# Kernel optimization log

Measured on AMD Instinct MI355X. Metric: run time of the kernel, lower is better.

The kernel has to match this reference:

```python
import jax, jax.numpy as jnp
import numpy as np
import math

B, L, E, H = 512, 200, 64, 4
D = E // H
NEG = jnp.float32(-(2.0 ** 32) + 1.0)


def setup_inputs() -> dict:
    key = jax.random.key(0)
    ks = jax.random.split(key, 12)
    inp = jax.random.normal(ks[0], (B, L, E), dtype=jnp.float32)
    # realistic variable-length histories: mask[b, t] = t < len_b, len_b in [1, L]
    lens = jax.random.randint(ks[1], (B, 1), 1, L + 1)
    mask = jnp.arange(L)[None, :] < lens  # [B, L] bool
    s = 1.0 / math.sqrt(E)
    pos_enc = jax.random.normal(ks[2], (1, L, E), dtype=jnp.float32)
    Wk = jax.random.uniform(ks[3], (E, E), jnp.float32, -s, s)
    bk = jnp.zeros((E,), jnp.float32)
    Wv = jax.random.uniform(ks[4], (E, E), jnp.float32, -s, s)
    bv = jnp.zeros((E,), jnp.float32)
    Wq = jax.random.uniform(ks[5], (E, E), jnp.float32, -s, s)
    bq = jnp.zeros((E,), jnp.float32)
    Wf = jax.random.uniform(ks[6], (E, E), jnp.float32, -s, s)
    bf = jnp.zeros((E,), jnp.float32)
    return {"input": inp, "mask": mask, "pos_enc": pos_enc,
            "Wk": Wk, "bk": bk, "Wv": Wv, "bv": bv,
            "Wq": Wq, "bq": bq, "Wf": Wf, "bf": bf}


def reference(input, mask, pos_enc, Wk, bk, Wv, bv, Wq, bq, Wf, bf):
    x = input + pos_enc  # [B, L, E]
    # project and split heads: [B, H, L, D]
    def split(t):
        return t.reshape(B, L, H, D).transpose(0, 2, 1, 3)
    k = split(x @ Wk.T + bk)
    v = split(x @ Wv.T + bv)
    q = split(x @ Wq.T + bq) / math.sqrt(D)
    scores = jnp.einsum('bhqd,bhkd->bhqk', q, k)  # [B, H, L, L]
    # key_mask in torch code broadcasts over dim 3 (mask on the QUERY axis),
    # query_mask is its transpose (mask on the KEY axis). Combined: both must be valid.
    both = mask[:, None, :, None] & mask[:, None, None, :]  # [B, 1, L, L]
    scores = jnp.where(both, scores, NEG)
    attn = jax.nn.softmax(scores, axis=-1)
    # dropout is identity at inference; omitted deterministically
    out = jnp.einsum('bhqk,bhkd->bhqd', attn, v)
    out = out.transpose(0, 2, 1, 3).reshape(B, L, E)
    out = out @ Wf.T + bf
    fm = mask.astype(jnp.float32)[:, :, None]  # [B, L, 1]
    lens = jnp.sum(fm, axis=1)  # [B, 1]
    pooled = jnp.sum(out * fm, axis=1) / (lens + 1e-8)  # [B, E]
    return pooled
```

## Files before the change

### kernel.cpp

```cpp
#include <hip/hip_runtime.h>
#include <hip/hip_fp16.h>
#include <math.h>

#define Bn 512
#define Ln 200
#define En 64
#define Hn 4
#define Dn 16
#define KS3 18
#define VS3 200
#define QSC 0.36067376022224085f

typedef _Float16 __f16;
typedef __f16 f16x4 __attribute__((ext_vector_type(4)));
typedef __f16 f16x8 __attribute__((ext_vector_type(8)));
typedef float f32x4 __attribute__((ext_vector_type(4)));

#if __has_builtin(__builtin_amdgcn_exp2f)
__device__ __forceinline__ float fexp2(float x) { return __builtin_amdgcn_exp2f(x); }
#else
__device__ __forceinline__ float fexp2(float x) { return exp2f(x); }
#endif

__device__ __forceinline__ f16x8 pack8s(float4 a, float4 b, float4 pa, float4 pb) {
    f16x8 r;
    r[0] = (__f16)(a.x + pa.x); r[1] = (__f16)(a.y + pa.y);
    r[2] = (__f16)(a.z + pa.z); r[3] = (__f16)(a.w + pa.w);
    r[4] = (__f16)(b.x + pb.x); r[5] = (__f16)(b.y + pb.y);
    r[6] = (__f16)(b.z + pb.z); r[7] = (__f16)(b.w + pb.w);
    return r;
}
__device__ __forceinline__ f16x8 pack8(float4 a, float4 b) {
    f16x8 r;
    r[0] = (__f16)a.x; r[1] = (__f16)a.y; r[2] = (__f16)a.z; r[3] = (__f16)a.w;
    r[4] = (__f16)b.x; r[5] = (__f16)b.y; r[6] = (__f16)b.z; r[7] = (__f16)b.w;
    return r;
}

__global__ __launch_bounds__(256, 4) void fused_kernel(
    const float* __restrict__ input, const int* __restrict__ mask,
    const float* __restrict__ pos_enc,
    const float* __restrict__ Wk, const float* __restrict__ bk,
    const float* __restrict__ Wv, const float* __restrict__ bv,
    const float* __restrict__ Wq, const float* __restrict__ bq,
    const float* __restrict__ Wf, const float* __restrict__ bf_,
    float* __restrict__ out)
{
    __shared__ __align__(16) __f16 Kh[Ln * KS3];
    __shared__ __align__(16) __f16 Qh[Ln * KS3];
    __shared__ __align__(16) __f16 Vt[16 * VS3];
    __shared__ float lred[4][4][16];
    __shared__ float red[4][16];
    __shared__ float ph[16];
    __shared__ int cnt_red[4];

    const int tid  = threadIdx.x;
    const int b    = blockIdx.x >> 2, h = blockIdx.x & 3;
    const int wave = tid >> 6, lane = tid & 63;
    const int quad = lane >> 4, ln16 = lane & 15;

    const int mv = (tid < Ln) ? mask[b * Ln + tid] : 0;

    f16x8 bfr[3][2];
    #pragma unroll
    for (int m = 0; m < 3; ++m) {
        const float* W = (m == 0) ? Wk : (m == 1) ? Wv : Wq;
        #pragma unroll
        for (int ks = 0; ks < 2; ++ks) {
            const float4* wp = (const float4*)(W + (size_t)(h * 16 + ln16) * 64) + (ks * 8 + quad * 2);
            bfr[m][ks] = pack8(wp[0], wp[1]);
        }
    }
    const int cg = h * 16 + ln16;
    const float bkv = bk[cg], bvv = bv[cg], bqv = bq[cg];

    int c = (mv != 0) ? 1 : 0;
    #pragma unroll
    for (int off = 32; off; off >>= 1) c += __shfl_down(c, off, 64);
    if (lane == 0) cnt_red[wave] = c;
    __syncthreads();
    const int len = cnt_red[0] + cnt_red[1] + cnt_red[2] + cnt_red[3];
    const int nt = (len + 15) >> 4;

    const float4* in4 = (const float4*)(input + (size_t)b * Ln * En);
    const float4* pe4 = (const float4*)pos_enc;

    for (int rt = wave; rt < nt; rt += 4) {
        const int R = rt * 16 + ln16;
        const bool rok = (R < Ln);
        f16x8 af[2];
        #pragma unroll
        for (int ks = 0; ks < 2; ++ks) {
            float4 xa = {0,0,0,0}, xb = {0,0,0,0}, pa = {0,0,0,0}, pb = {0,0,0,0};
            if (rok) {
                const int o4 = R * 16 + ks * 8 + quad * 2;
                xa = in4[o4]; xb = in4[o4 + 1];
                pa = pe4[o4]; pb = pe4[o4 + 1];
            }
            af[ks] = pack8s(xa, xb, pa, pb);
        }
        f32x4 acc[3];
        #pragma unroll
        for (int m = 0; m < 3; ++m) acc[m] = (f32x4){0,0,0,0};
        #pragma unroll
        for (int ks = 0; ks < 2; ++ks)
            #pragma unroll
            for (int m = 0; m < 3; ++m)
                acc[m] = __builtin_amdgcn_mfma_f32_16x16x32_f16(af[ks], bfr[m][ks], acc[m], 0, 0, 0);

        #pragma unroll
        for (int j = 0; j < 4; ++j) {
            const int t = rt * 16 + quad * 4 + j;
            if (t < Ln) {
                Kh[t * KS3 + ln16] = (__f16)(acc[0][j] + bkv);
                Qh[t * KS3 + ln16] = (__f16)((acc[2][j] + bqv) * QSC);
            }
        }
        const int vc0 = rt * 16 + quad * 4;
        if (vc0 < Ln) {
            f16x4 vp;
            #pragma unroll
            for (int j = 0; j < 4; ++j) vp[j] = (__f16)(acc[1][j] + bvv);
            *(f16x4*)(Vt + ln16 * VS3 + vc0) = vp;
        }
    }
    __syncthreads();

    const int nquad = (nt + 3) >> 2;
    int g, kh, nkh;
    if (nquad >= 3)      { g = wave;     kh = 0;         nkh = 1; }
    else if (nquad == 2) { g = wave & 1; kh = wave >> 1; nkh = 2; }
    else                 { g = 0;        kh = wave;      nkh = 4; }
    const bool active = (g < nquad);
    const int nktp = (nt + nkh - 1) / nkh;
    const int klo = kh * nktp;
    const int khi = min(klo + nktp, nt);
    const int qt0 = 4 * g;

    const f16x4 ones = {(__f16)1.f, (__f16)1.f, (__f16)1.f, (__f16)1.f};
    f32x4 o2[4], lacc[4];
    #pragma unroll
    for (int i = 0; i < 4; ++i) { o2[i] = (f32x4){0,0,0,0}; lacc[i] = (f32x4){0,0,0,0}; }

    if (active && klo < khi) {
        f16x4 qf[4];
        #pragma unroll
        for (int i = 0; i < 4; ++i) {
            int qr = min((qt0 + i) * 16 + ln16, Ln - 1);
            qf[i] = *(const f16x4*)(Qh + qr * KS3 + quad * 4);
        }
        const bool needmask = (khi == nt);
        const int kfull = khi - (needmask ? 1 : 0);

        f16x4 kf = *(const f16x4*)(Kh + min(klo * 16 + ln16, Ln - 1) * KS3 + quad * 4);
        f16x4 vf = *(const f16x4*)(Vt + ln16 * VS3 + min(klo * 16 + quad * 4, Ln - 4));

        for (int kt = klo; kt < kfull; ++kt) {
            const int krn = min((kt + 1) * 16 + ln16, Ln - 1);
            const int vcn = min((kt + 1) * 16 + quad * 4, Ln - 4);
            const f16x4 kfn = *(const f16x4*)(Kh + krn * KS3 + quad * 4);
            const f16x4 vfn = *(const f16x4*)(Vt + ln16 * VS3 + vcn);
            f32x4 s[4];
            #pragma unroll
            for (int i = 0; i < 4; ++i)
                s[i] = __builtin_amdgcn_mfma_f32_16x16x16f16(kf, qf[i], (f32x4){0,0,0,0}, 0, 0, 0);
            f16x4 pf[4];
            #pragma unroll
            for (int i = 0; i < 4; ++i) {
                #pragma unroll
                for (int j = 0; j < 4; ++j)
                    pf[i][j] = (__f16)fexp2(fminf(s[i][j], 14.5f));
            }
            #pragma unroll
            for (int i = 0; i < 4; ++i) {
                o2[i]   = __builtin_amdgcn_mfma_f32_16x16x16f16(vf,   pf[i], o2[i],   0, 0, 0);
                lacc[i] = __builtin_amdgcn_mfma_f32_16x16x16f16(ones, pf[i], lacc[i], 0, 0, 0);
            }
            kf = kfn; vf = vfn;
        }
        if (needmask) {
            const int kbase = (nt - 1) * 16 + quad * 4;
            f32x4 s[4];
            #pragma unroll
            for (int i = 0; i < 4; ++i)
                s[i] = __builtin_amdgcn_mfma_f32_16x16x16f16(kf, qf[i], (f32x4){0,0,0,0}, 0, 0, 0);
            f16x4 pf[4];
            #pragma unroll
            for (int i = 0; i < 4; ++i) {
                #pragma unroll
                for (int j = 0; j < 4; ++j) {
                    const bool kok = (kbase + j) < len;
                    pf[i][j] = kok ? (__f16)fexp2(fminf(s[i][j], 14.5f)) : (__f16)0.f;
                }
            }
            #pragma unroll
            for (int i = 0; i < 4; ++i) {
                o2[i]   = __builtin_amdgcn_mfma_f32_16x16x16f16(vf,   pf[i], o2[i],   0, 0, 0);
                lacc[i] = __builtin_amdgcn_mfma_f32_16x16x16f16(ones, pf[i], lacc[i], 0, 0, 0);
            }
        }
    }

    float l[4];
    #pragma unroll
    for (int i = 0; i < 4; ++i) l[i] = lacc[i][0];

    if (nkh > 1) {
        if (lane < 16) {
            #pragma unroll
            for (int i = 0; i < 4; ++i) lred[wave][i][lane] = l[i];
        }
        __syncthreads();
        #pragma unroll
        for (int i = 0; i < 4; ++i) {
            if (nkh == 2) l[i] = lred[g][i][ln16] + lred[g + 2][i][ln16];
            else          l[i] = lred[0][i][ln16] + lred[1][i][ln16]
                               + lred[2][i][ln16] + lred[3][i][ln16];
        }
    }

    f32x4 pool = {0.f, 0.f, 0.f, 0.f};
    if (active) {
        #pragma unroll
        for (int i = 0; i < 4; ++i) {
            const float rs = ((qt0 + i) * 16 + ln16 < len) ? 1.f / l[i] : 0.f;
            #pragma unroll
            for (int j = 0; j < 4; ++j) pool[j] = fmaf(o2[i][j], rs, pool[j]);
        }
    }

    #pragma unroll
    for (int j = 0; j < 4; ++j) {
        #pragma unroll
        for (int off = 1; off < 16; off <<= 1) pool[j] += __shfl_xor(pool[j], off, 64);
    }
    if (ln16 == 0) {
        #pragma unroll
        for (int j = 0; j < 4; ++j) red[wave][quad * 4 + j] = pool[j];
    }
    __syncthreads();
    if (tid < 16)
        ph[tid] = (red[0][tid] + red[1][tid] + red[2][tid] + red[3][tid]) / ((float)len + 1e-8f);
    __syncthreads();

    if (tid < 64) {
        const int e = tid;
        const float* wr = Wf + (size_t)e * 64 + h * 16;
        float a = (h == 0) ? bf_[e] : 0.f;
        #pragma unroll
        for (int i = 0; i < 16; ++i) a = fmaf(wr[i], ph[i], a);
        atomicAdd(out + b * En + e, a);
    }
}

extern "C" void kernel_launch(void* const* d_in, const int* in_sizes, int n_in,
                              void* d_out, int out_size, void* d_ws, size_t ws_size,
                              hipStream_t stream) {
    const float* input   = (const float*)d_in[0];
    const int*   mask    = (const int*)  d_in[1];
    const float* pos_enc = (const float*)d_in[2];
    const float* Wk      = (const float*)d_in[3];
    const float* bk      = (const float*)d_in[4];
    const float* Wv      = (const float*)d_in[5];
    const float* bv      = (const float*)d_in[6];
    const float* Wq      = (const float*)d_in[7];
    const float* bq      = (const float*)d_in[8];
    const float* Wf      = (const float*)d_in[9];
    const float* bf      = (const float*)d_in[10];

    float* out = (float*)d_out;
    hipMemsetAsync(out, 0, (size_t)Bn * En * sizeof(float), stream);

    fused_kernel<<<Bn * Hn, 256, 0, stream>>>(input, mask, pos_enc,
                                              Wk, bk, Wv, bv, Wq, bq, Wf, bf, out);
}
```

Measured before the change: 122.3 us.

## Keep Q in registers, project all tiles up front, drop key-split scheduling

Each wave now loads its four row tiles and projects them before the length reduction, so the global loads no longer wait on the mask count. Q is produced directly in MFMA fragment layout through an operand swap and kept in registers, which removes the Qh shared buffer and its round trip. The adaptive key-split scheme and its lred reduction are removed, so each wave owns fixed query tiles. In exchange, every block projects all 13 tiles even for short sequences, short sequences lose key-split parallelism, and the occupancy hint drops from 4 to 3 blocks per SIMD.

```diff
diff --git a/kernel.cpp b/kernel.cpp
--- a/kernel.cpp
+++ b/kernel.cpp
@@ -7,6 +7,7 @@
 #define En 64
 #define Hn 4
 #define Dn 16
+#define NT13 13
 #define KS3 18
 #define VS3 200
 #define QSC 0.36067376022224085f
@@ -37,7 +38,7 @@
     return r;
 }
 
-__global__ __launch_bounds__(256, 4) void fused_kernel(
+__global__ __launch_bounds__(256, 3) void fused_kernel(
     const float* __restrict__ input, const int* __restrict__ mask,
     const float* __restrict__ pos_enc,
     const float* __restrict__ Wk, const float* __restrict__ bk,
@@ -47,9 +48,7 @@
     float* __restrict__ out)
 {
     __shared__ __align__(16) __f16 Kh[Ln * KS3];
-    __shared__ __align__(16) __f16 Qh[Ln * KS3];
     __shared__ __align__(16) __f16 Vt[16 * VS3];
-    __shared__ float lred[4][4][16];
     __shared__ float red[4][16];
     __shared__ float ph[16];
     __shared__ int cnt_red[4];
@@ -61,34 +60,14 @@
 
     const int mv = (tid < Ln) ? mask[b * Ln + tid] : 0;
 
-    f16x8 bfr[3][2];
-    #pragma unroll
-    for (int m = 0; m < 3; ++m) {
-        const float* W = (m == 0) ? Wk : (m == 1) ? Wv : Wq;
-        #pragma unroll
-        for (int ks = 0; ks < 2; ++ks) {
-            const float4* wp = (const float4*)(W + (size_t)(h * 16 + ln16) * 64) + (ks * 8 + quad * 2);
-            bfr[m][ks] = pack8(wp[0], wp[1]);
-        }
-    }
-    const int cg = h * 16 + ln16;
-    const float bkv = bk[cg], bvv = bv[cg], bqv = bq[cg];
-
-    int c = (mv != 0) ? 1 : 0;
-    #pragma unroll
-    for (int off = 32; off; off >>= 1) c += __shfl_down(c, off, 64);
-    if (lane == 0) cnt_red[wave] = c;
-    __syncthreads();
-    const int len = cnt_red[0] + cnt_red[1] + cnt_red[2] + cnt_red[3];
-    const int nt = (len + 15) >> 4;
-
     const float4* in4 = (const float4*)(input + (size_t)b * Ln * En);
     const float4* pe4 = (const float4*)pos_enc;
-
-    for (int rt = wave; rt < nt; rt += 4) {
-        const int R = rt * 16 + ln16;
-        const bool rok = (R < Ln);
-        f16x8 af[2];
+    f16x8 af[4][2];
+    #pragma unroll
+    for (int i = 0; i < 4; ++i) {
+        const int rt = 4 * wave + i;
+        const int R  = rt * 16 + ln16;
+        const bool rok = (rt < NT13) && (R < Ln);
         #pragma unroll
         for (int ks = 0; ks < 2; ++ks) {
             float4 xa = {0,0,0,0}, xb = {0,0,0,0}, pa = {0,0,0,0}, pb = {0,0,0,0};
@@ -97,65 +76,76 @@
                 xa = in4[o4]; xb = in4[o4 + 1];
                 pa = pe4[o4]; pb = pe4[o4 + 1];
             }
-            af[ks] = pack8s(xa, xb, pa, pb);
-        }
-        f32x4 acc[3];
-        #pragma unroll
-        for (int m = 0; m < 3; ++m) acc[m] = (f32x4){0,0,0,0};
-        #pragma unroll
-        for (int ks = 0; ks < 2; ++ks)
-            #pragma unroll
-            for (int m = 0; m < 3; ++m)
-                acc[m] = __builtin_amdgcn_mfma_f32_16x16x32_f16(af[ks], bfr[m][ks], acc[m], 0, 0, 0);
-
-        #pragma unroll
-        for (int j = 0; j < 4; ++j) {
-            const int t = rt * 16 + quad * 4 + j;
-            if (t < Ln) {
-                Kh[t * KS3 + ln16] = (__f16)(acc[0][j] + bkv);
-                Qh[t * KS3 + ln16] = (__f16)((acc[2][j] + bqv) * QSC);
-            }
-        }
-        const int vc0 = rt * 16 + quad * 4;
-        if (vc0 < Ln) {
-            f16x4 vp;
-            #pragma unroll
-            for (int j = 0; j < 4; ++j) vp[j] = (__f16)(acc[1][j] + bvv);
-            *(f16x4*)(Vt + ln16 * VS3 + vc0) = vp;
-        }
-    }
+            af[i][ks] = pack8s(xa, xb, pa, pb);
+        }
+    }
+
+    f16x8 bfr[3][2];
+    #pragma unroll
+    for (int m = 0; m < 3; ++m) {
+        const float* W = (m == 0) ? Wk : (m == 1) ? Wv : Wq;
+        #pragma unroll
+        for (int ks = 0; ks < 2; ++ks) {
+            const float4* wp = (const float4*)(W + (size_t)(h * 16 + ln16) * 64) + (ks * 8 + quad * 2);
+            bfr[m][ks] = pack8(wp[0], wp[1]);
+        }
+    }
+    const int cg = h * 16 + ln16;
+    const float bkv = bk[cg], bvv = bv[cg];
+    const float4 bq4 = ((const float4*)bq)[h * 4 + quad];
+
+    f16x4 qf[4];
+    #pragma unroll
+    for (int i = 0; i < 4; ++i) {
+        const int rt = 4 * wave + i;
+        if (rt < NT13) {
+            f32x4 ak = {0,0,0,0}, av = {0,0,0,0}, aq = {0,0,0,0};
+            #pragma unroll
+            for (int ks = 0; ks < 2; ++ks) {
+                ak = __builtin_amdgcn_mfma_f32_16x16x32_f16(af[i][ks], bfr[0][ks], ak, 0, 0, 0);
+                av = __builtin_amdgcn_mfma_f32_16x16x32_f16(af[i][ks], bfr[1][ks], av, 0, 0, 0);
+                aq = __builtin_amdgcn_mfma_f32_16x16x32_f16(bfr[2][ks], af[i][ks], aq, 0, 0, 0);
+            }
+            #pragma unroll
+            for (int j = 0; j < 4; ++j) {
+                const int t = rt * 16 + quad * 4 + j;
+                if (t < Ln) Kh[t * KS3 + ln16] = (__f16)(ak[j] + bkv);
+            }
+            const int vc0 = rt * 16 + quad * 4;
+            if (vc0 < Ln) {
+                f16x4 vp;
+                #pragma unroll
+                for (int j = 0; j < 4; ++j) vp[j] = (__f16)(av[j] + bvv);
+                *(f16x4*)(Vt + ln16 * VS3 + vc0) = vp;
+            }
+            qf[i][0] = (__f16)((aq[0] + bq4.x) * QSC);
+            qf[i][1] = (__f16)((aq[1] + bq4.y) * QSC);
+            qf[i][2] = (__f16)((aq[2] + bq4.z) * QSC);
+            qf[i][3] = (__f16)((aq[3] + bq4.w) * QSC);
+        } else {
+            qf[i] = (f16x4){(__f16)0.f, (__f16)0.f, (__f16)0.f, (__f16)0.f};
+        }
+    }
+
+    int c = (mv != 0) ? 1 : 0;
+    #pragma unroll
+    for (int off = 32; off; off >>= 1) c += __shfl_down(c, off, 64);
+    if (lane == 0) cnt_red[wave] = c;
     __syncthreads();
-
-    const int nquad = (nt + 3) >> 2;
-    int g, kh, nkh;
-    if (nquad >= 3)      { g = wave;     kh = 0;         nkh = 1; }
-    else if (nquad == 2) { g = wave & 1; kh = wave >> 1; nkh = 2; }
-    else                 { g = 0;        kh = wave;      nkh = 4; }
-    const bool active = (g < nquad);
-    const int nktp = (nt + nkh - 1) / nkh;
-    const int klo = kh * nktp;
-    const int khi = min(klo + nktp, nt);
-    const int qt0 = 4 * g;
-
+    const int len = cnt_red[0] + cnt_red[1] + cnt_red[2] + cnt_red[3];
+    const int nt = (len + 15) >> 4;
+
+    const bool active = (4 * wave < nt);
     const f16x4 ones = {(__f16)1.f, (__f16)1.f, (__f16)1.f, (__f16)1.f};
     f32x4 o2[4], lacc[4];
     #pragma unroll
     for (int i = 0; i < 4; ++i) { o2[i] = (f32x4){0,0,0,0}; lacc[i] = (f32x4){0,0,0,0}; }
 
-    if (active && klo < khi) {
-        f16x4 qf[4];
-        #pragma unroll
-        for (int i = 0; i < 4; ++i) {
-            int qr = min((qt0 + i) * 16 + ln16, Ln - 1);
-            qf[i] = *(const f16x4*)(Qh + qr * KS3 + quad * 4);
-        }
-        const bool needmask = (khi == nt);
-        const int kfull = khi - (needmask ? 1 : 0);
-
-        f16x4 kf = *(const f16x4*)(Kh + min(klo * 16 + ln16, Ln - 1) * KS3 + quad * 4);
-        f16x4 vf = *(const f16x4*)(Vt + ln16 * VS3 + min(klo * 16 + quad * 4, Ln - 4));
-
-        for (int kt = klo; kt < kfull; ++kt) {
+    if (active) {
+        f16x4 kf = *(const f16x4*)(Kh + ln16 * KS3 + quad * 4);
+        f16x4 vf = *(const f16x4*)(Vt + ln16 * VS3 + quad * 4);
+
+        for (int kt = 0; kt < nt - 1; ++kt) {
             const int krn = min((kt + 1) * 16 + ln16, Ln - 1);
             const int vcn = min((kt + 1) * 16 + quad * 4, Ln - 4);
             const f16x4 kfn = *(const f16x4*)(Kh + krn * KS3 + quad * 4);
@@ -178,7 +168,7 @@
             }
             kf = kfn; vf = vfn;
         }
-        if (needmask) {
+        {
             const int kbase = (nt - 1) * 16 + quad * 4;
             f32x4 s[4];
             #pragma unroll
@@ -201,29 +191,11 @@
         }
     }
 
-    float l[4];
-    #pragma unroll
-    for (int i = 0; i < 4; ++i) l[i] = lacc[i][0];
-
-    if (nkh > 1) {
-        if (lane < 16) {
-            #pragma unroll
-            for (int i = 0; i < 4; ++i) lred[wave][i][lane] = l[i];
-        }
-        __syncthreads();
-        #pragma unroll
-        for (int i = 0; i < 4; ++i) {
-            if (nkh == 2) l[i] = lred[g][i][ln16] + lred[g + 2][i][ln16];
-            else          l[i] = lred[0][i][ln16] + lred[1][i][ln16]
-                               + lred[2][i][ln16] + lred[3][i][ln16];
-        }
-    }
-
     f32x4 pool = {0.f, 0.f, 0.f, 0.f};
     if (active) {
         #pragma unroll
         for (int i = 0; i < 4; ++i) {
-            const float rs = ((qt0 + i) * 16 + ln16 < len) ? 1.f / l[i] : 0.f;
+            const float rs = ((4 * wave + i) * 16 + ln16 < len) ? 1.f / lacc[i][0] : 0.f;
             #pragma unroll
             for (int j = 0; j < 4; ++j) pool[j] = fmaf(o2[i][j], rs, pool[j]);
         }
```

After: 131.1 us. 7.2% more time.
